# Performance work log

Hardware: AMD Instinct MI355X
Metric: run time of the kernel (lower is better)

## Reference

```python
import jax, jax.numpy as jnp
import numpy as np

N = 524288   # total points across all events
H = 128      # MLP hidden width
B = 1024     # number of batches (events)


def setup_inputs() -> dict:
    key = jax.random.key(0)
    ks = jax.random.split(key, 6)
    # features[:,0] = per-point input mean, features[:,1] = per-point input std (>0)
    mean = jax.random.normal(ks[0], (N, 1), dtype=jnp.float32)
    std = jax.random.uniform(ks[1], (N, 1), dtype=jnp.float32) * 0.5 + 0.1
    features = jnp.concatenate([mean, std], axis=1)            # [N,2]
    batch_ids = jax.random.randint(ks[2], (N,), 0, B).astype(jnp.int32)
    s = 1.0 / np.sqrt(H).astype(np.float32)
    W1 = jax.random.normal(ks[3], (1, H), dtype=jnp.float32)
    b1 = jnp.zeros((H,), jnp.float32)
    W2 = jax.random.normal(ks[4], (H, H), dtype=jnp.float32) * s
    b2 = jnp.zeros((H,), jnp.float32)
    W3 = jax.random.normal(ks[5], (H, 1), dtype=jnp.float32) * s
    b3 = jnp.zeros((1,), jnp.float32)
    return {"features": features, "batch_ids": batch_ids,
            "W1": W1, "b1": b1, "W2": W2, "b2": b2, "W3": W3, "b3": b3,
            "num_batches": B}


def reference(features, batch_ids, W1, b1, W2, b2, W3, b3, num_batches):
    x0 = features[:, :1]        # [N,1] input means (x.features in the original)
    inpt_std = features[:, 1]   # [N]   input stds
    n = x0.shape[0]
    counts = jnp.maximum(
        jax.ops.segment_sum(jnp.ones((n,), x0.dtype), batch_ids,
                            num_segments=num_batches), 1.0)      # [B]

    def net(x):
        # pointwise MLP then global average pool per batch -> one scalar per event
        h = jnp.tanh(x @ W1 + b1)        # [N,H]
        h = jnp.tanh(h @ W2 + b2)        # [N,H]
        s = (h @ W3 + b3)[:, 0]          # [N]
        return jax.ops.segment_sum(s, batch_ids, num_segments=num_batches) / counts  # [B]

    pred_mean, vjp_fn = jax.vjp(net, x0)
    # d pred[b] / d x_j is nonzero only for points j in batch b (pointwise net +
    # per-batch pool), so ONE VJP with a ones cotangent yields every per-batch
    # Jacobian row simultaneously -- collapsing the original per-batch
    # torch.autograd.grad loop into a single backward pass.
    jac = vjp_fn(jnp.ones_like(pred_mean))[0][:, 0]              # [N]
    # var_b = jac_b^T diag(std_b^2) jac_b = sum_{j in b} std_j^2 * jac_j^2
    pred_sdp_var = jax.ops.segment_sum(inpt_std ** 2 * jac ** 2, batch_ids,
                                       num_segments=num_batches)  # [B]
    return jnp.stack([pred_mean, pred_sdp_var], axis=1)           # [B,2]
```

## Files before the change

### kernel.cpp

```cpp
#include <hip/hip_runtime.h>


#define HH   128
#define NB   1024
#define TBL  4096
#define XMIN (-8.0f)
#define XMAX (8.0f)

__global__ __launch_bounds__(256) void zero_acc_kernel(float* __restrict__ acc) {
    int i = blockIdx.x * 256 + threadIdx.x;
    if (i < 3 * NB) acc[i] = 0.0f;
}

__global__ __launch_bounds__(256) void build_table_kernel(
    const float* __restrict__ W1, const float* __restrict__ b1,
    const float* __restrict__ W2, const float* __restrict__ b2,
    const float* __restrict__ W3, const float* __restrict__ b3,
    float* __restrict__ s_tab, float* __restrict__ d_tab)
{
    __shared__ float W2s[HH * HH];
    __shared__ float h1s[8][HH];
    __shared__ float us[8][HH];
    const int tid = threadIdx.x;
    {
        const float4* src = (const float4*)W2;
        float4* dst = (float4*)W2s;
        for (int i = tid; i < HH * HH / 4; i += 256) dst[i] = src[i];
    }
    const int e = tid >> 5;
    const int q = tid & 31;
    const float dxt = (XMAX - XMIN) / (float)(TBL - 1);
    const int eg = blockIdx.x * 8 + e;
    const float x = XMIN + (float)eg * dxt;
    #pragma unroll
    for (int kk = 0; kk < 4; ++kk) {
        int k = q * 4 + kk;
        float w1 = W1[k];
        float h = tanhf(fmaf(x, w1, b1[k]));
        h1s[e][k] = h;
        us[e][k] = w1 * (1.0f - h * h);
    }
    __syncthreads();

    float accz[4] = {0.f, 0.f, 0.f, 0.f};
    float accv[4] = {0.f, 0.f, 0.f, 0.f};
    const int jb = q * 4;
    #pragma unroll 2
    for (int k = 0; k < HH; k += 4) {
        float4 h4 = *(const float4*)&h1s[e][k];
        float4 u4 = *(const float4*)&us[e][k];
        float hk[4] = {h4.x, h4.y, h4.z, h4.w};
        float uk[4] = {u4.x, u4.y, u4.z, u4.w};
        #pragma unroll
        for (int kk = 0; kk < 4; ++kk) {
            float4 w = *(const float4*)&W2s[(k + kk) * HH + jb];
            float h = hk[kk], u = uk[kk];
            accz[0] = fmaf(h, w.x, accz[0]); accv[0] = fmaf(u, w.x, accv[0]);
            accz[1] = fmaf(h, w.y, accz[1]); accv[1] = fmaf(u, w.y, accv[1]);
            accz[2] = fmaf(h, w.z, accz[2]); accv[2] = fmaf(u, w.z, accv[2]);
            accz[3] = fmaf(h, w.w, accz[3]); accv[3] = fmaf(u, w.w, accv[3]);
        }
    }
    float ps = 0.f, pd = 0.f;
    #pragma unroll
    for (int i = 0; i < 4; ++i) {
        int j = jb + i;
        float h2 = tanhf(accz[i] + b2[j]);
        float w3 = W3[j];
        ps = fmaf(w3, h2, ps);
        pd = fmaf((1.0f - h2 * h2) * w3, accv[i], pd);
    }
    #pragma unroll
    for (int o = 16; o > 0; o >>= 1) {
        ps += __shfl_down(ps, o, 32);
        pd += __shfl_down(pd, o, 32);
    }
    if (q == 0) {
        s_tab[eg] = ps + b3[0];
        d_tab[eg] = pd;
    }
}

__device__ __forceinline__ float catmull(const float* __restrict__ tab, int i0, float t) {
    float fm = tab[i0 - 1], f0 = tab[i0], f1 = tab[i0 + 1], f2 = tab[i0 + 2];
    float a1 = 0.5f * (f1 - fm);
    float a2 = fm - 2.5f * f0 + 2.0f * f1 - 0.5f * f2;
    float a3 = 1.5f * (f0 - f1) + 0.5f * (f2 - fm);
    return fmaf(fmaf(fmaf(a3, t, a2), t, a1), t, f0);
}

__global__ __launch_bounds__(256) void main_pass_kernel(
    const float2* __restrict__ feat, const int* __restrict__ ids,
    const float* __restrict__ s_tab, const float* __restrict__ d_tab,
    float* __restrict__ acc, int n)
{
    __shared__ float bs[NB];
    __shared__ float bv[NB];
    __shared__ float bc[NB];
    const int tid = threadIdx.x;
    for (int i = tid; i < NB; i += 256) { bs[i] = 0.f; bv[i] = 0.f; bc[i] = 0.f; }
    __syncthreads();
    const float inv_dx = (float)(TBL - 1) / (XMAX - XMIN);
    const int stride = gridDim.x * 256;
    for (int i = blockIdx.x * 256 + tid; i < n; i += stride) {
        float2 f = feat[i];
        int b = ids[i];
        float x = fminf(fmaxf(f.x, XMIN), XMAX);
        float u = (x - XMIN) * inv_dx;
        int i0 = (int)u;
        i0 = min(max(i0, 1), TBL - 3);
        float t = u - (float)i0;
        float s = catmull(s_tab, i0, t);
        float d = catmull(d_tab, i0, t);
        atomicAdd(&bs[b], s);
        atomicAdd(&bv[b], f.y * f.y * d * d);
        atomicAdd(&bc[b], 1.0f);
    }
    __syncthreads();
    for (int b = tid; b < NB; b += 256) {
        float c = bc[b];
        if (c != 0.f) {
            atomicAdd(&acc[b], bs[b]);
            atomicAdd(&acc[NB + b], bv[b]);
            atomicAdd(&acc[2 * NB + b], c);
        }
    }
}

__global__ __launch_bounds__(256) void finalize_kernel(const float* __restrict__ acc,
                                                       float* __restrict__ out) {
    int b = blockIdx.x * 256 + threadIdx.x;
    if (b < NB) {
        float c = fmaxf(acc[2 * NB + b], 1.0f);
        out[2 * b]     = acc[b] / c;
        out[2 * b + 1] = acc[NB + b] / (c * c);
    }
}

extern "C" void kernel_launch(void* const* d_in, const int* in_sizes, int n_in,
                              void* d_out, int out_size, void* d_ws, size_t ws_size,
                              hipStream_t stream) {
    const float* feat = (const float*)d_in[0];
    const int*   ids  = (const int*)d_in[1];
    const float* W1   = (const float*)d_in[2];
    const float* b1   = (const float*)d_in[3];
    const float* W2   = (const float*)d_in[4];
    const float* b2   = (const float*)d_in[5];
    const float* W3   = (const float*)d_in[6];
    const float* b3   = (const float*)d_in[7];
    const int n = in_sizes[1];

    float* s_tab = (float*)d_ws;
    float* d_tab = s_tab + TBL;
    float* acc   = d_tab + TBL;

    zero_acc_kernel<<<(3 * NB + 255) / 256, 256, 0, stream>>>(acc);
    build_table_kernel<<<TBL / 8, 256, 0, stream>>>(W1, b1, W2, b2, W3, b3, s_tab, d_tab);
    main_pass_kernel<<<256, 256, 0, stream>>>((const float2*)feat, ids, s_tab, d_tab, acc, n);
    finalize_kernel<<<(NB + 255) / 256, 256, 0, stream>>>(acc, (float*)d_out);
}
```

Before: 99.89 us.

## Fuse zero and finalize kernels, interleave tables, compute two entries per warp

Removes the separate zero and finalize launches: block 0 of the table build zeroes the accumulators and a done counter, and the last main-pass block (found with an atomic ticket) writes the normalized output. The s and d tables are interleaved into float2 so each lookup fetches paired values. The table build now handles 16 entries per block, with each warp computing two entries per W2 load to reuse weights from shared memory. This cuts launch overhead and table-build work, at the cost of a grid-wide last-block pattern that depends on correct fences.

```diff
diff --git a/kernel.cpp b/kernel.cpp
--- a/kernel.cpp
+++ b/kernel.cpp
@@ -6,83 +6,85 @@
 #define TBL  4096
 #define XMIN (-8.0f)
 #define XMAX (8.0f)
-
-__global__ __launch_bounds__(256) void zero_acc_kernel(float* __restrict__ acc) {
-    int i = blockIdx.x * 256 + threadIdx.x;
-    if (i < 3 * NB) acc[i] = 0.0f;
-}
+#define EPB  16
+#define BUILD_BLOCKS (TBL / EPB)
+#define MAIN_BLOCKS  256
 
 __global__ __launch_bounds__(256) void build_table_kernel(
     const float* __restrict__ W1, const float* __restrict__ b1,
     const float* __restrict__ W2, const float* __restrict__ b2,
     const float* __restrict__ W3, const float* __restrict__ b3,
-    float* __restrict__ s_tab, float* __restrict__ d_tab)
+    float2* __restrict__ tab2, float* __restrict__ acc, unsigned* __restrict__ done)
 {
     __shared__ float W2s[HH * HH];
-    __shared__ float h1s[8][HH];
-    __shared__ float us[8][HH];
+    __shared__ float hus[HH * 2 * EPB];
     const int tid = threadIdx.x;
     {
         const float4* src = (const float4*)W2;
         float4* dst = (float4*)W2s;
         for (int i = tid; i < HH * HH / 4; i += 256) dst[i] = src[i];
     }
-    const int e = tid >> 5;
-    const int q = tid & 31;
+    if (blockIdx.x == 0) {
+        for (int i = tid; i < 3 * NB; i += 256) acc[i] = 0.0f;
+        if (tid == 0) *done = 0u;
+    }
     const float dxt = (XMAX - XMIN) / (float)(TBL - 1);
-    const int eg = blockIdx.x * 8 + e;
-    const float x = XMIN + (float)eg * dxt;
-    #pragma unroll
-    for (int kk = 0; kk < 4; ++kk) {
-        int k = q * 4 + kk;
+    const int ebase = blockIdx.x * EPB;
+    for (int i = tid; i < EPB * HH; i += 256) {
+        int e = i & (EPB - 1);
+        int k = i >> 4;
+        float x = XMIN + (float)(ebase + e) * dxt;
         float w1 = W1[k];
         float h = tanhf(fmaf(x, w1, b1[k]));
-        h1s[e][k] = h;
-        us[e][k] = w1 * (1.0f - h * h);
+        hus[k * (2 * EPB) + 2 * e]     = h;
+        hus[k * (2 * EPB) + 2 * e + 1] = w1 * (1.0f - h * h);
     }
     __syncthreads();
 
-    float accz[4] = {0.f, 0.f, 0.f, 0.f};
-    float accv[4] = {0.f, 0.f, 0.f, 0.f};
+    const int q = tid & 31;
+    const int r = tid >> 5;
     const int jb = q * 4;
-    #pragma unroll 2
-    for (int k = 0; k < HH; k += 4) {
-        float4 h4 = *(const float4*)&h1s[e][k];
-        float4 u4 = *(const float4*)&us[e][k];
-        float hk[4] = {h4.x, h4.y, h4.z, h4.w};
-        float uk[4] = {u4.x, u4.y, u4.z, u4.w};
-        #pragma unroll
-        for (int kk = 0; kk < 4; ++kk) {
-            float4 w = *(const float4*)&W2s[(k + kk) * HH + jb];
-            float h = hk[kk], u = uk[kk];
-            accz[0] = fmaf(h, w.x, accz[0]); accv[0] = fmaf(u, w.x, accv[0]);
-            accz[1] = fmaf(h, w.y, accz[1]); accv[1] = fmaf(u, w.y, accv[1]);
-            accz[2] = fmaf(h, w.z, accz[2]); accv[2] = fmaf(u, w.z, accv[2]);
-            accz[3] = fmaf(h, w.w, accz[3]); accv[3] = fmaf(u, w.w, accv[3]);
-        }
+    float z0[4] = {0,0,0,0}, v0[4] = {0,0,0,0};
+    float z1[4] = {0,0,0,0}, v1[4] = {0,0,0,0};
+    #pragma unroll 4
+    for (int k = 0; k < HH; ++k) {
+        float4 w  = *(const float4*)&W2s[k * HH + jb];
+        float4 hu = *(const float4*)&hus[k * (2 * EPB) + 4 * r];
+        z0[0] = fmaf(hu.x, w.x, z0[0]); z0[1] = fmaf(hu.x, w.y, z0[1]);
+        z0[2] = fmaf(hu.x, w.z, z0[2]); z0[3] = fmaf(hu.x, w.w, z0[3]);
+        v0[0] = fmaf(hu.y, w.x, v0[0]); v0[1] = fmaf(hu.y, w.y, v0[1]);
+        v0[2] = fmaf(hu.y, w.z, v0[2]); v0[3] = fmaf(hu.y, w.w, v0[3]);
+        z1[0] = fmaf(hu.z, w.x, z1[0]); z1[1] = fmaf(hu.z, w.y, z1[1]);
+        z1[2] = fmaf(hu.z, w.z, z1[2]); z1[3] = fmaf(hu.z, w.w, z1[3]);
+        v1[0] = fmaf(hu.w, w.x, v1[0]); v1[1] = fmaf(hu.w, w.y, v1[1]);
+        v1[2] = fmaf(hu.w, w.z, v1[2]); v1[3] = fmaf(hu.w, w.w, v1[3]);
     }
-    float ps = 0.f, pd = 0.f;
+    float ps0 = 0.f, pd0 = 0.f, ps1 = 0.f, pd1 = 0.f;
     #pragma unroll
     for (int i = 0; i < 4; ++i) {
         int j = jb + i;
-        float h2 = tanhf(accz[i] + b2[j]);
-        float w3 = W3[j];
-        ps = fmaf(w3, h2, ps);
-        pd = fmaf((1.0f - h2 * h2) * w3, accv[i], pd);
+        float b2j = b2[j], w3 = W3[j];
+        float h2 = tanhf(z0[i] + b2j);
+        ps0 = fmaf(w3, h2, ps0);
+        pd0 = fmaf((1.0f - h2 * h2) * w3, v0[i], pd0);
+        float h2b = tanhf(z1[i] + b2j);
+        ps1 = fmaf(w3, h2b, ps1);
+        pd1 = fmaf((1.0f - h2b * h2b) * w3, v1[i], pd1);
     }
     #pragma unroll
     for (int o = 16; o > 0; o >>= 1) {
-        ps += __shfl_down(ps, o, 32);
-        pd += __shfl_down(pd, o, 32);
+        ps0 += __shfl_down(ps0, o, 32); pd0 += __shfl_down(pd0, o, 32);
+        ps1 += __shfl_down(ps1, o, 32); pd1 += __shfl_down(pd1, o, 32);
     }
     if (q == 0) {
-        s_tab[eg] = ps + b3[0];
-        d_tab[eg] = pd;
+        float bb = b3[0];
+        int e = ebase + 2 * r;
+        tab2[e]     = make_float2(ps0 + bb, pd0);
+        tab2[e + 1] = make_float2(ps1 + bb, pd1);
     }
 }
 
-__device__ __forceinline__ float catmull(const float* __restrict__ tab, int i0, float t) {
-    float fm = tab[i0 - 1], f0 = tab[i0], f1 = tab[i0 + 1], f2 = tab[i0 + 2];
+__device__ __forceinline__ float cm(float fm, float f0, float f1, float f2, float t) {
     float a1 = 0.5f * (f1 - fm);
     float a2 = fm - 2.5f * f0 + 2.0f * f1 - 0.5f * f2;
     float a3 = 1.5f * (f0 - f1) + 0.5f * (f2 - fm);
@@ -91,27 +93,28 @@
 
 __global__ __launch_bounds__(256) void main_pass_kernel(
     const float2* __restrict__ feat, const int* __restrict__ ids,
-    const float* __restrict__ s_tab, const float* __restrict__ d_tab,
-    float* __restrict__ acc, int n)
+    const float2* __restrict__ tab2, float* __restrict__ acc,
+    unsigned* __restrict__ done, float* __restrict__ out, int n)
 {
     __shared__ float bs[NB];
     __shared__ float bv[NB];
     __shared__ float bc[NB];
+    __shared__ int lastflag;
     const int tid = threadIdx.x;
     for (int i = tid; i < NB; i += 256) { bs[i] = 0.f; bv[i] = 0.f; bc[i] = 0.f; }
     __syncthreads();
     const float inv_dx = (float)(TBL - 1) / (XMAX - XMIN);
-    const int stride = gridDim.x * 256;
+    const int stride = MAIN_BLOCKS * 256;
     for (int i = blockIdx.x * 256 + tid; i < n; i += stride) {
         float2 f = feat[i];
         int b = ids[i];
-        float x = fminf(fmaxf(f.x, XMIN), XMAX);
-        float u = (x - XMIN) * inv_dx;
+        float u = (fminf(fmaxf(f.x, XMIN), XMAX) - XMIN) * inv_dx;
         int i0 = (int)u;
         i0 = min(max(i0, 1), TBL - 3);
         float t = u - (float)i0;
-        float s = catmull(s_tab, i0, t);
-        float d = catmull(d_tab, i0, t);
+        float2 fm = tab2[i0 - 1], f0 = tab2[i0], f1 = tab2[i0 + 1], f2 = tab2[i0 + 2];
+        float s = cm(fm.x, f0.x, f1.x, f2.x, t);
+        float d = cm(fm.y, f0.y, f1.y, f2.y, t);
         atomicAdd(&bs[b], s);
         atomicAdd(&bv[b], f.y * f.y * d * d);
         atomicAdd(&bc[b], 1.0f);
@@ -125,15 +128,26 @@
             atomicAdd(&acc[2 * NB + b], c);
         }
     }
-}
-
-__global__ __launch_bounds__(256) void finalize_kernel(const float* __restrict__ acc,
-                                                       float* __restrict__ out) {
-    int b = blockIdx.x * 256 + threadIdx.x;
-    if (b < NB) {
-        float c = fmaxf(acc[2 * NB + b], 1.0f);
-        out[2 * b]     = acc[b] / c;
-        out[2 * b + 1] = acc[NB + b] / (c * c);
+    __threadfence();
+    __syncthreads();
+    if (tid == 0) {
+        unsigned old = __hip_atomic_fetch_add(done, 1u, __ATOMIC_ACQ_REL,
+                                              __HIP_MEMORY_SCOPE_AGENT);
+        lastflag = (old == (unsigned)(MAIN_BLOCKS - 1)) ? 1 : 0;
+    }
+    __syncthreads();
+    if (lastflag) {
+        for (int b = tid; b < NB; b += 256) {
+            float ssum = __hip_atomic_load(&acc[b], __ATOMIC_RELAXED,
+                                           __HIP_MEMORY_SCOPE_AGENT);
+            float vsum = __hip_atomic_load(&acc[NB + b], __ATOMIC_RELAXED,
+                                           __HIP_MEMORY_SCOPE_AGENT);
+            float c = __hip_atomic_load(&acc[2 * NB + b], __ATOMIC_RELAXED,
+                                        __HIP_MEMORY_SCOPE_AGENT);
+            c = fmaxf(c, 1.0f);
+            out[2 * b]     = ssum / c;
+            out[2 * b + 1] = vsum / (c * c);
+        }
     }
 }
 
@@ -150,12 +164,13 @@
     const float* b3   = (const float*)d_in[7];
     const int n = in_sizes[1];
 
-    float* s_tab = (float*)d_ws;
-    float* d_tab = s_tab + TBL;
-    float* acc   = d_tab + TBL;
+    float2*   tab2 = (float2*)d_ws;
+    float*    acc  = (float*)(tab2 + TBL);
+    unsigned* done = (unsigned*)(acc + 3 * NB);
 
-    zero_acc_kernel<<<(3 * NB + 255) / 256, 256, 0, stream>>>(acc);
-    build_table_kernel<<<TBL / 8, 256, 0, stream>>>(W1, b1, W2, b2, W3, b3, s_tab, d_tab);
-    main_pass_kernel<<<256, 256, 0, stream>>>((const float2*)feat, ids, s_tab, d_tab, acc, n);
-    finalize_kernel<<<(NB + 255) / 256, 256, 0, stream>>>(acc, (float*)d_out);
+    build_table_kernel<<<BUILD_BLOCKS, 256, 0, stream>>>(W1, b1, W2, b2, W3, b3,
+                                                         tab2, acc, done);
+    main_pass_kernel<<<MAIN_BLOCKS, 256, 0, stream>>>((const float2*)feat, ids,
+                                                      tab2, acc, done,
+                                                      (float*)d_out, n);
 }
```

Result: slower. 116.3 us (+16.4%).
